# Performance work log

Hardware: AMD Instinct MI355X
Metric: run time of the kernel (lower is better)

## Reference

```python
import jax, jax.numpy as jnp
import numpy as np

EPS = 1e-8
NEG = -1e7  # min_val used by masked_max


def _div_safe(a, b):
    return a / jnp.maximum(b, EPS)


def _masked_max(v, m, axis):
    mb = jnp.broadcast_to(m, v.shape)
    val = jnp.where(mb > 0, v, NEG).max(axis=axis)
    return val * mb.max(axis=axis)


def _masked_mean(v, m, axis):
    mb = jnp.broadcast_to(m, v.shape)
    return _div_safe((v * mb).sum(axis=axis), mb.sum(axis=axis))


def _cos_pairwise(v1, v2):
    # v1: (b,p,h), v2: (b,q,h) -> (b,p,q)
    n1 = jnp.linalg.norm(v1, axis=2, keepdims=True)
    n2 = jnp.linalg.norm(v2, axis=2, keepdims=True)
    dot = jnp.einsum('bph,bqh->bpq', v1, v2)
    return _div_safe(dot, n1 * n2.transpose(0, 2, 1))


def _mpm(v1, v2, w):
    # v1,v2: (b,L,h); w: (np,h) -> ((b,L,1), (b,L,np))
    dot = (v1 * v2).sum(-1)
    n = jnp.linalg.norm(v1, axis=-1) * jnp.linalg.norm(v2, axis=-1)
    mv1 = _div_safe(dot, n)[..., None]
    wv1 = w[None, None] * v1[:, :, None, :]  # (b,L,np,h)
    wv2 = w[None, None] * v2[:, :, None, :]
    dotm = (wv1 * wv2).sum(-1)
    nm = jnp.linalg.norm(wv1, axis=-1) * jnp.linalg.norm(wv2, axis=-1)
    return mv1, _div_safe(dotm, nm)


def _mpm_pairwise(v1, v2, w):
    # v1: (b,L1,h), v2: (b,L2,h), w: (np,h) -> (b,L1,L2,np)
    wv1 = w[None, :, None, :] * v1[:, None, :, :]  # (b,np,L1,h)
    wv2 = w[None, :, None, :] * v2[:, None, :, :]  # (b,np,L2,h)
    n1 = jnp.linalg.norm(wv1, axis=3, keepdims=True)
    n2 = jnp.linalg.norm(wv2, axis=3, keepdims=True)
    dot = jnp.einsum('bnph,bnqh->bnpq', wv1, wv2)
    res = _div_safe(dot, n1 * n2.transpose(0, 1, 3, 2))
    return res.transpose(0, 2, 3, 1)


def _bimpm(context_p, mask_p, context_h, mask_h, w_full, w_maxpool, w_att, w_max_att):
    b = context_p.shape[0]
    mask_p_h = mask_p[:, :, None] * mask_h[:, None, :]  # (b,Lp,Lh)
    mask_h_p = mask_p_h.transpose(0, 2, 1)
    context_p = context_p * mask_p[:, :, None]
    context_h = context_h * mask_h[:, :, None]

    cos = _cos_pairwise(context_p, context_h)  # (b,Lp,Lh)
    mv_p = [_masked_max(cos, mask_p_h, 2)[:, :, None],
            _masked_mean(cos, mask_p_h, 2)[:, :, None]]
    cos_t = cos.transpose(0, 2, 1)
    mv_h = [_masked_max(cos_t, mask_h_p, 2)[:, :, None],
            _masked_mean(cos_t, mask_h_p, 2)[:, :, None]]

    # full match (is_forward=True): match against last non-pad token
    idx_p = jnp.clip(mask_p.sum(1).astype(jnp.int32) - 1, 0)
    idx_h = jnp.clip(mask_h.sum(1).astype(jnp.int32) - 1, 0)
    last_p = context_p[jnp.arange(b), idx_p][:, None, :]  # (b,1,h)
    last_h = context_h[jnp.arange(b), idx_h][:, None, :]
    m1, mm = _mpm(context_p, jnp.broadcast_to(last_h, context_p.shape), w_full)
    mv_p += [m1, mm]
    m1, mm = _mpm(context_h, jnp.broadcast_to(last_p, context_h.shape), w_full)
    mv_h += [m1, mm]

    # maxpool match
    mv_max = _mpm_pairwise(context_p, context_h, w_maxpool)  # (b,Lp,Lh,np)
    mv_p += [_masked_max(mv_max, mask_p_h[..., None], 2),
             _masked_mean(mv_max, mask_p_h[..., None], 2)]
    mv_max_t = mv_max.transpose(0, 2, 1, 3)
    mv_h += [_masked_max(mv_max_t, mask_h_p[..., None], 2),
             _masked_mean(mv_max_t, mask_h_p[..., None], 2)]

    # attentive match
    att_h = context_h[:, None, :, :] * cos[..., None]  # (b,Lp,Lh,h)
    att_p = context_p[:, :, None, :] * cos[..., None]  # (b,Lp,Lh,h)
    att_mean_h = _div_safe(jnp.einsum('bpq,bqh->bph', cos, context_h),
                           cos.sum(2, keepdims=True))
    att_mean_p = _div_safe(jnp.einsum('bpq,bph->bqh', cos, context_p),
                           cos.sum(1, keepdims=True).transpose(0, 2, 1))
    m1, mm = _mpm(context_p, att_mean_h, w_att)
    mv_p += [m1, mm]
    m1, mm = _mpm(context_h, att_mean_p, w_att)
    mv_h += [m1, mm]

    # max attentive match
    att_max_h = _masked_max(att_h, mask_p_h[..., None], 2)  # (b,Lp,h)
    att_max_p = _masked_max(att_p.transpose(0, 2, 1, 3), mask_h_p[..., None], 2)  # (b,Lh,h)
    m1, mm = _mpm(context_p, att_max_h, w_max_att)
    mv_p += [m1, mm]
    m1, mm = _mpm(context_h, att_max_p, w_max_att)
    mv_h += [m1, mm]

    return jnp.concatenate(mv_p, axis=2), jnp.concatenate(mv_h, axis=2)


def setup_inputs() -> dict:
    B, LP, LH, H, NP = 32, 128, 128, 200, 20
    key = jax.random.key(0)
    ks = jax.random.split(key, 8)
    len_p = jax.random.randint(ks[0], (B,), LP // 2, LP + 1)
    len_h = jax.random.randint(ks[1], (B,), LH // 2, LH + 1)
    return {
        'context_p': jax.random.normal(ks[2], (B, LP, H), dtype=jnp.float32),
        'mask_p': (jnp.arange(LP)[None, :] < len_p[:, None]).astype(jnp.float32),
        'context_h': jax.random.normal(ks[3], (B, LH, H), dtype=jnp.float32),
        'mask_h': (jnp.arange(LH)[None, :] < len_h[:, None]).astype(jnp.float32),
        'w_full': jax.random.uniform(ks[4], (NP, H), dtype=jnp.float32),
        'w_maxpool': jax.random.uniform(ks[5], (NP, H), dtype=jnp.float32),
        'w_att': jax.random.uniform(ks[6], (NP, H), dtype=jnp.float32),
        'w_max_att': jax.random.uniform(ks[7], (NP, H), dtype=jnp.float32),
    }


def reference(context_p, mask_p, context_h, mask_h, w_full, w_maxpool, w_att, w_max_att):
    return _bimpm(context_p, mask_p, context_h, mask_h, w_full, w_maxpool, w_att, w_max_att)
```

## Files before the change

### kernel.cpp

```cpp
#include <hip/hip_runtime.h>
#include <hip/hip_bf16.h>


#define EPSF 1e-8f
#define NEGF -1e7f

constexpr int Bc = 32, Lc = 128, Hc = 200, NPc = 20, NCHc = 105;
constexpr int KP = 224;
constexpr size_t SLH = (size_t)Bc * Lc * Hc;
constexpr size_t SLL = (size_t)Bc * Lc * Lc;

constexpr size_t OFF_CPM    = 0;
constexpr size_t OFF_CHM    = OFF_CPM + SLH;
constexpr size_t OFF_CHMT   = OFF_CHM + SLH;
constexpr size_t OFF_COS    = OFF_CHMT + SLH;
constexpr size_t OFF_COST   = OFF_COS + SLL;
constexpr size_t OFF_AMEANH = OFF_COST + SLL;
constexpr size_t OFF_AMAXH  = OFF_AMEANH + SLH;
constexpr size_t OFF_AMEANP = OFF_AMAXH + SLH;
constexpr size_t OFF_AMAXP  = OFF_AMEANP + SLH;
constexpr size_t OFF_NORMP  = OFF_AMAXP + SLH;
constexpr size_t OFF_NORMH  = OFF_NORMP + (size_t)Bc * Lc;
constexpr size_t OFF_LENP   = OFF_NORMH + (size_t)Bc * Lc;
constexpr size_t OFF_LENH   = OFF_LENP + Bc;
constexpr size_t OFF_LASTP  = OFF_LENH + Bc;
constexpr size_t OFF_LASTH  = OFF_LASTP + (size_t)Bc * Hc;
constexpr size_t OFF_NWP    = OFF_LASTH + (size_t)Bc * Hc;
constexpr size_t OFF_NWH    = OFF_NWP + (size_t)Bc * NPc * Lc;
constexpr size_t OFF_MASKPF = OFF_NWH + (size_t)Bc * NPc * Lc;
constexpr size_t OFF_MASKHF = OFF_MASKPF + (size_t)Bc * Lc;
constexpr size_t OFF_WFULL  = OFF_MASKHF + (size_t)Bc * Lc;
constexpr size_t OFF_WMP    = OFF_WFULL + (size_t)NPc * Hc;
constexpr size_t OFF_WATT   = OFF_WMP + (size_t)NPc * Hc;
constexpr size_t OFF_WMATT  = OFF_WATT + (size_t)NPc * Hc;
constexpr size_t OFF_FLAG   = OFF_WMATT + (size_t)NPc * Hc;
constexpr size_t OFF_WT     = OFF_FLAG + 64;
constexpr size_t OFF_RPMAX  = OFF_WT + (size_t)Hc * 64;
constexpr size_t OFF_RPSUM  = OFF_RPMAX + 2 * (size_t)Bc * NPc * Lc;
constexpr size_t OFF_CPMAX  = OFF_RPSUM + 2 * (size_t)Bc * NPc * Lc;
constexpr size_t OFF_CPSUM  = OFF_CPMAX + 2 * (size_t)Bc * NPc * Lc;
constexpr size_t OFF_CHB    = OFF_CPSUM + 2 * (size_t)Bc * NPc * Lc;
constexpr size_t OFF_CPB    = OFF_CHB + ((size_t)Bc * Lc * KP) / 2;
constexpr size_t OFF_W2K    = OFF_CPB + ((size_t)Bc * Lc * KP) / 2;
constexpr size_t WS_FLOATS  = OFF_W2K + (size_t)NPc * KP;

typedef __attribute__((ext_vector_type(8))) short short8v;
typedef __attribute__((ext_vector_type(4))) short short4v;
typedef __attribute__((ext_vector_type(4))) float float4v;

__device__ __forceinline__ float loadf(const void* p, size_t i, int isb) {
  if (isb) return __bfloat162float(((const __hip_bfloat16*)p)[i]);
  return ((const float*)p)[i];
}

__device__ __forceinline__ void storef(void* out, size_t i, float v, int isb) {
  if (isb) ((__hip_bfloat16*)out)[i] = __float2bfloat16(v);
  else ((float*)out)[i] = v;
}

__device__ __forceinline__ short b2s(float f) {
  __hip_bfloat16 h = __float2bfloat16(f);
  union { __hip_bfloat16 b; short s; } u;
  u.b = h;
  return u.s;
}

__device__ __forceinline__ short8v weight8(short8v a, float4v w0, float4v w1) {
  short8v r;
#pragma unroll
  for (int e = 0; e < 8; e++) {
    union { unsigned u; float f; } c;
    c.u = ((unsigned)(unsigned short)a[e]) << 16;
    float w = (e < 4) ? w0[e] : w1[e - 4];
    r[e] = b2s(c.f * w);
  }
  return r;
}

__global__ void convert_kernel(const void* cp_, const void* mp, const void* ch_,
                               const void* mh, const void* wf, const void* wmp,
                               const void* watt, const void* wma,
                               float* __restrict__ ws) {
  int isb = (((const unsigned short*)mp)[0] == 0x3F80u) ? 1 : 0;
  int bid = blockIdx.x;
  const int n0 = Bc * Lc;
  const int nw = NPc * Hc;
  if (bid >= 162) {
    int t = threadIdx.x;
    int idx = (bid - 162) * 4 + (t >> 6);
    int side = idx >> 5, b = idx & 31;
    int lane = t & 63;
    const void* mask = side ? mh : mp;
    const void* ctx = side ? ch_ : cp_;
    float s = 0.f;
    for (int l = lane; l < Lc; l += 64) s += loadf(mask, b * Lc + l, isb);
    for (int o = 32; o > 0; o >>= 1) s += __shfl_xor(s, o);
    if (lane == 0) ws[(side ? OFF_LENH : OFF_LENP) + b] = s;
    int lidx = (int)(s + 0.5f) - 1;
    if (lidx < 0) lidx = 0;
    float mk = loadf(mask, b * Lc + lidx, isb);
    float* lastv = ws + (side ? OFF_LASTH : OFF_LASTP) + (size_t)b * Hc;
    for (int h = lane; h < Hc; h += 64)
      lastv[h] = loadf(ctx, ((size_t)b * Lc + lidx) * Hc + h, isb) * mk;
    return;
  }
  int g = bid * 256 + threadIdx.x;
  if (g == 0) ws[OFF_FLAG] = (float)isb;
  if (g < n0) {
    ws[OFF_MASKPF + g] = loadf(mp, g, isb);
  } else if (g < 2 * n0) {
    ws[OFF_MASKHF + (g - n0)] = loadf(mh, g - n0, isb);
  } else if (g < 2 * n0 + 4 * nw) {
    int r = g - 2 * n0;
    int seg = r / nw, off = r % nw;
    if (seg == 0) ws[OFF_WFULL + off] = loadf(wf, off, isb);
    else if (seg == 1) ws[OFF_WMP + off] = loadf(wmp, off, isb);
    else if (seg == 2) ws[OFF_WATT + off] = loadf(watt, off, isb);
    else ws[OFF_WMATT + off] = loadf(wma, off, isb);
  } else if (g < 2 * n0 + 4 * nw + 64 * Hc) {
    int r = g - (2 * n0 + 4 * nw);
    int c = r / Hc, h = r % Hc;
    float w = 1.0f;
    if (c < 20) w = loadf(wf, (size_t)c * Hc + h, isb);
    else if (c < 40) w = loadf(watt, (size_t)(c - 20) * Hc + h, isb);
    else if (c < 60) w = loadf(wma, (size_t)(c - 40) * Hc + h, isb);
    ws[OFF_WT + r] = w * w;
  } else if (g < 2 * n0 + 4 * nw + 64 * Hc + NPc * KP) {
    int r = g - (2 * n0 + 4 * nw + 64 * Hc);
    int np_ = r / KP, k = r % KP;
    float w = (k < Hc) ? loadf(wmp, (size_t)np_ * Hc + k, isb) : 0.f;
    ws[OFF_W2K + r] = w * w;
  }
}

__global__ void prep_kernel(const void* __restrict__ ctx_p,
                            const void* __restrict__ ctx_h,
                            float* __restrict__ ws) {
  int bid = blockIdx.x;
  int side = bid >> 12;
  int bl = bid & 4095;
  int b = bl >> 7, l = bl & 127;
  int lane = threadIdx.x;
  int isb = ws[OFF_FLAG] > 0.5f;
  const void* ctx = side ? ctx_h : ctx_p;
  const float* mask = ws + (side ? OFF_MASKHF : OFF_MASKPF);
  float mk = mask[b * Lc + l];
  size_t rowbase = ((size_t)b * Lc + l) * Hc;
  float* cm = ws + (side ? OFF_CHM : OFF_CPM) + rowbase;
  __hip_bfloat16* cb16 = (__hip_bfloat16*)(ws + (side ? OFF_CHB : OFF_CPB));
  size_t cb = ((size_t)b * Lc + l) * KP;

  float v[4];
  float ss = 0.f;
  for (int i = 0; i < 4; i++) {
    int h = lane + 64 * i;
    float x = 0.f;
    if (h < Hc) {
      x = loadf(ctx, rowbase + h, isb) * mk;
      cm[h] = x;
      cb16[cb + h] = __float2bfloat16(x);
    } else if (h < KP) {
      cb16[cb + h] = __float2bfloat16(0.f);
    }
    v[i] = x;
    ss += x * x;
  }
  for (int o = 32; o > 0; o >>= 1) ss += __shfl_xor(ss, o);
  if (lane == 0) ws[(side ? OFF_NORMH : OFF_NORMP) + b * Lc + l] = sqrtf(ss);

  const float* wmpf = ws + OFF_WMP;
  float* nw = ws + (side ? OFF_NWH : OFF_NWP) + (size_t)b * NPc * Lc;
  for (int np_ = 0; np_ < NPc; np_++) {
    float s = 0.f;
    for (int i = 0; i < 4; i++) {
      int h = lane + 64 * i;
      if (h < Hc) {
        float w = wmpf[np_ * Hc + h];
        float wx = w * v[i];
        s += wx * wx;
      }
    }
    for (int o = 32; o > 0; o >>= 1) s += __shfl_xor(s, o);
    if (lane == 0) nw[np_ * Lc + l] = sqrtf(s);
  }
}

__global__ __launch_bounds__(64, 3) void maxpool_kernel(float* __restrict__ ws) {
  int s = blockIdx.x;
  int np_ = blockIdx.y, b = blockIdx.z;
  int pi = s >> 1, qi = s & 1;
  int cosmode = (np_ == NPc);
  int lane = threadIdx.x;
  int rsel = lane & 15, quad = lane >> 4;

  const short* Ab = (const short*)(ws + OFF_CPB)
                  + ((size_t)b * Lc + pi * 64 + rsel) * KP + quad * 8;
  const short* Bb = (const short*)(ws + OFF_CHB)
                  + ((size_t)b * Lc + qi * 64 + rsel) * KP + quad * 8;
  const float* w2k = ws + OFF_W2K + (size_t)(cosmode ? 0 : np_) * KP + quad * 8;

  float4v acc[4][4];
  float4v zf = {0.f, 0.f, 0.f, 0.f};
#pragma unroll
  for (int i = 0; i < 4; i++)
#pragma unroll
    for (int j = 0; j < 4; j++) acc[i][j] = zf;

#pragma unroll
  for (int st = 0; st < 7; st++) {
    int k0 = st * 32;
    short8v bf4[4], af[4];
#pragma unroll
    for (int t = 0; t < 4; t++)
      bf4[t] = *(const short8v*)(Bb + (size_t)t * 16 * KP + k0);
    if (cosmode) {
#pragma unroll
      for (int t = 0; t < 4; t++)
        af[t] = *(const short8v*)(Ab + (size_t)t * 16 * KP + k0);
    } else {
      float4v w0 = *(const float4v*)(w2k + k0);
      float4v w1 = *(const float4v*)(w2k + k0 + 4);
#pragma unroll
      for (int t = 0; t < 4; t++) {
        short8v ar = *(const short8v*)(Ab + (size_t)t * 16 * KP + k0);
        af[t] = weight8(ar, w0, w1);
      }
    }
#pragma unroll
    for (int i = 0; i < 4; i++)
#pragma unroll
      for (int j = 0; j < 4; j++)
        acc[i][j] = __builtin_amdgcn_mfma_f32_16x16x32_bf16(af[i], bf4[j], acc[i][j], 0, 0, 0);
  }

  if (cosmode) {
    const float* npn = ws + OFF_NORMP + b * Lc + pi * 64;
    const float* nhn = ws + OFF_NORMH + b * Lc + qi * 64;
    float nh4[4];
#pragma unroll
    for (int tj = 0; tj < 4; tj++) nh4[tj] = nhn[tj * 16 + rsel];
    float* cosp = ws + OFF_COS + (size_t)b * Lc * Lc;
    float* cost = ws + OFF_COST + (size_t)b * Lc * Lc;
#pragma unroll
    for (int ti = 0; ti < 4; ti++) {
#pragma unroll
      for (int r = 0; r < 4; r++) {
        int prow = pi * 64 + ti * 16 + quad * 4 + r;
        float npv = npn[ti * 16 + quad * 4 + r];
#pragma unroll
        for (int tj = 0; tj < 4; tj++) {
          int qcol = qi * 64 + tj * 16 + rsel;
          float v = acc[ti][tj][r] * __builtin_amdgcn_rcpf(fmaxf(npv * nh4[tj], EPSF));
          cosp[(size_t)prow * Lc + qcol] = v;
          cost[(size_t)qcol * Lc + prow] = v;
        }
      }
    }
    return;
  }

  const float* nwp = ws + OFF_NWP + ((size_t)b * NPc + np_) * Lc + pi * 64;
  const float* nwh = ws + OFF_NWH + ((size_t)b * NPc + np_) * Lc + qi * 64;
  const float* maskP = ws + OFF_MASKPF + b * Lc + pi * 64;
  const float* maskH = ws + OFF_MASKHF + b * Lc + qi * 64;
  float nhv[4], mhv[4], cmax[4], csum[4];
#pragma unroll
  for (int tj = 0; tj < 4; tj++) {
    int q = tj * 16 + rsel;
    nhv[tj] = nwh[q];
    mhv[tj] = maskH[q];
    cmax[tj] = NEGF;
    csum[tj] = 0.f;
  }
  size_t rbase = (((size_t)qi * Bc + b) * NPc + np_) * Lc + pi * 64;
  size_t cbase = (((size_t)pi * Bc + b) * NPc + np_) * Lc + qi * 64;
#pragma unroll
  for (int ti = 0; ti < 4; ti++) {
#pragma unroll
    for (int r = 0; r < 4; r++) {
      int p = ti * 16 + quad * 4 + r;
      float npv = nwp[p], mpv = maskP[p];
      float rm = NEGF, rs = 0.f;
#pragma unroll
      for (int tj = 0; tj < 4; tj++) {
        float v = acc[ti][tj][r] * __builtin_amdgcn_rcpf(fmaxf(npv * nhv[tj], EPSF));
        if (mhv[tj] > 0.f) rm = fmaxf(rm, v);
        rs += v * mhv[tj];
        if (mpv > 0.f) cmax[tj] = fmaxf(cmax[tj], v);
        csum[tj] += v * mpv;
      }
#pragma unroll
      for (int o = 1; o <= 8; o <<= 1) {
        rm = fmaxf(rm, __shfl_xor(rm, o));
        rs += __shfl_xor(rs, o);
      }
      if (rsel == 0) {
        ws[OFF_RPMAX + rbase + p] = rm;
        ws[OFF_RPSUM + rbase + p] = rs;
      }
    }
  }
#pragma unroll
  for (int tj = 0; tj < 4; tj++) {
#pragma unroll
    for (int o = 16; o <= 32; o <<= 1) {
      cmax[tj] = fmaxf(cmax[tj], __shfl_xor(cmax[tj], o));
      csum[tj] += __shfl_xor(csum[tj], o);
    }
  }
  if (quad == 0) {
#pragma unroll
    for (int tj = 0; tj < 4; tj++) {
      int q = tj * 16 + rsel;
      ws[OFF_CPMAX + cbase + q] = cmax[tj];
      ws[OFF_CPSUM + cbase + q] = csum[tj];
    }
  }
}

__global__ __launch_bounds__(256) void att_kernel(float* __restrict__ ws,
                                                  void* __restrict__ out) {
  int side = blockIdx.z;
  int b = blockIdx.y;
  int r0 = blockIdx.x * 4;
  int t = threadIdx.x;
  int isb = ws[OFF_FLAG] > 0.5f;
  const float* cosrows = ws + (side ? OFF_COST : OFF_COS) + ((size_t)b * Lc + r0) * Lc;
  const float* vsrc = ws + (side ? OFF_CPM : OFF_CHM) + (size_t)b * Lc * Hc;
  const float* maskLoop = ws + (side ? OFF_MASKPF : OFF_MASKHF) + b * Lc;
  const float* maskRow = ws + (side ? OFF_MASKHF : OFF_MASKPF) + b * Lc;
  float lenOther = ws[(side ? OFF_LENP : OFF_LENH) + b];
  float* amean = ws + (side ? OFF_AMEANP : OFF_AMEANH) + ((size_t)b * Lc + r0) * Hc;
  float* amax = ws + (side ? OFF_AMAXP : OFF_AMAXH) + ((size_t)b * Lc + r0) * Hc;

  __shared__ float crow[4][Lc];
  __shared__ float mneg[Lc];
  __shared__ float dens[4];
  for (int i = t; i < 4 * Lc; i += 256) crow[i >> 7][i & 127] = cosrows[i];
  if (t < Lc) mneg[t] = (maskLoop[t] > 0.f) ? 0.f : -1e30f;
  __syncthreads();

  int wv = t >> 6, lane = t & 63;
  {
    float x1 = crow[wv][lane], x2 = crow[wv][lane + 64];
    float sv = x1 + x2;
    float mv = fmaxf(x1 + mneg[lane], x2 + mneg[lane + 64]);
    for (int o = 32; o > 0; o >>= 1) {
      sv += __shfl_xor(sv, o);
      mv = fmaxf(mv, __shfl_xor(mv, o));
    }
    if (lane == 0) {
      dens[wv] = sv;
      float mr = maskRow[r0 + wv];
      size_t orow = (size_t)side * Bc * Lc * NCHc + ((size_t)b * Lc + r0 + wv) * NCHc;
      storef(out, orow + 0, mr * mv, isb);
      storef(out, orow + 1, mr * sv / fmaxf(mr * lenOther, EPSF), isb);
    }
  }
  __syncthreads();

  if (t < Hc) {
    float s0 = 0.f, s1 = 0.f, s2 = 0.f, s3 = 0.f;
    float m0 = NEGF, m1 = NEGF, m2 = NEGF, m3 = NEGF;
    const float* vb = vsrc + t;
#pragma unroll 4
    for (int q = 0; q < Lc; q++) {
      float pr = vb[(size_t)q * Hc];
      float mn = mneg[q];
      float v0 = crow[0][q] * pr; s0 += v0; m0 = fmaxf(m0, v0 + mn);
      float v1 = crow[1][q] * pr; s1 += v1; m1 = fmaxf(m1, v1 + mn);
      float v2 = crow[2][q] * pr; s2 += v2; m2 = fmaxf(m2, v2 + mn);
      float v3 = crow[3][q] * pr; s3 += v3; m3 = fmaxf(m3, v3 + mn);
    }
    amean[0 * Hc + t] = s0 / fmaxf(dens[0], EPSF);
    amean[1 * Hc + t] = s1 / fmaxf(dens[1], EPSF);
    amean[2 * Hc + t] = s2 / fmaxf(dens[2], EPSF);
    amean[3 * Hc + t] = s3 / fmaxf(dens[3], EPSF);
    amax[0 * Hc + t] = maskRow[r0 + 0] * m0;
    amax[1 * Hc + t] = maskRow[r0 + 1] * m1;
    amax[2 * Hc + t] = maskRow[r0 + 2] * m2;
    amax[3 * Hc + t] = maskRow[r0 + 3] * m3;
  }
}

__global__ __launch_bounds__(64) void mpm_kernel(float* __restrict__ ws,
                                                 void* __restrict__ out) {
  int bid = blockIdx.x;
  int side = bid >> 11;
  int b = (bid >> 6) & 31;
  int l0 = (bid & 63) * 2;
  int c = threadIdx.x;
  int isb = ws[OFF_FLAG] > 0.5f;
  __shared__ float v1s[2][Hc], v2l[Hc], v2a[2][Hc], v2m[2][Hc];
  const float* v1 = ws + (side ? OFF_CHM : OFF_CPM) + ((size_t)b * Lc + l0) * Hc;
  const float* vlast = ws + (side ? OFF_LASTP : OFF_LASTH) + (size_t)b * Hc;
  const float* va = ws + (side ? OFF_AMEANP : OFF_AMEANH) + ((size_t)b * Lc + l0) * Hc;
  const float* vm = ws + (side ? OFF_AMAXP : OFF_AMAXH) + ((size_t)b * Lc + l0) * Hc;
  for (int h = c; h < Hc; h += 64) {
    v1s[0][h] = v1[h];
    v1s[1][h] = v1[h + Hc];
    v2l[h] = vlast[h];
    v2a[0][h] = va[h];
    v2a[1][h] = va[h + Hc];
    v2m[0][h] = vm[h];
    v2m[1][h] = vm[h + Hc];
  }
  if (c < NPc) {
    size_t PMX = side ? OFF_CPMAX : OFF_RPMAX;
    size_t PSM = side ? OFF_CPSUM : OFF_RPSUM;
    float len = ws[(side ? OFF_LENP : OFF_LENH) + b];
#pragma unroll
    for (int l = 0; l < 2; l++) {
      size_t i0 = (((size_t)0 * Bc + b) * NPc + c) * Lc + l0 + l;
      size_t i1 = (((size_t)1 * Bc + b) * NPc + c) * Lc + l0 + l;
      float m = fmaxf(ws[PMX + i0], ws[PMX + i1]);
      float sum = ws[PSM + i0] + ws[PSM + i1];
      float mk = ws[(side ? OFF_MASKHF : OFF_MASKPF) + b * Lc + l0 + l];
      size_t orow = (size_t)side * Bc * Lc * NCHc + ((size_t)b * Lc + l0 + l) * NCHc;
      storef(out, orow + 23 + c, mk * m, isb);
      storef(out, orow + 43 + c, mk * sum / fmaxf(mk * len, EPSF), isb);
    }
  }
  __syncthreads();
  int v2i = (c < 20) ? 0 : (c < 40) ? 1 : (c < 60) ? 2 : (c - 60);
  if (v2i > 2) v2i = 2;
  const float* y0 = (v2i == 0) ? v2l : (v2i == 1) ? v2a[0] : v2m[0];
  const float* y1 = (v2i == 0) ? v2l : (v2i == 1) ? v2a[1] : v2m[1];
  const float* wt = ws + OFF_WT + (size_t)c * Hc;
  float sd0 = 0.f, sa0 = 0.f, sb0 = 0.f;
  float sd1 = 0.f, sa1 = 0.f, sb1 = 0.f;
#pragma unroll 2
  for (int h4 = 0; h4 < Hc / 4; h4++) {
    float4 wq = *(const float4*)(wt + h4 * 4);
    float4 x0 = *(const float4*)&v1s[0][h4 * 4];
    float4 x1 = *(const float4*)&v1s[1][h4 * 4];
    float4 ya = *(const float4*)&y0[h4 * 4];
    float4 yb = *(const float4*)&y1[h4 * 4];
    float t0;
    t0 = wq.x * x0.x; sd0 += t0 * ya.x; sa0 += t0 * x0.x; sb0 += wq.x * ya.x * ya.x;
    t0 = wq.y * x0.y; sd0 += t0 * ya.y; sa0 += t0 * x0.y; sb0 += wq.y * ya.y * ya.y;
    t0 = wq.z * x0.z; sd0 += t0 * ya.z; sa0 += t0 * x0.z; sb0 += wq.z * ya.z * ya.z;
    t0 = wq.w * x0.w; sd0 += t0 * ya.w; sa0 += t0 * x0.w; sb0 += wq.w * ya.w * ya.w;
    t0 = wq.x * x1.x; sd1 += t0 * yb.x; sa1 += t0 * x1.x; sb1 += wq.x * yb.x * yb.x;
    t0 = wq.y * x1.y; sd1 += t0 * yb.y; sa1 += t0 * x1.y; sb1 += wq.y * yb.y * yb.y;
    t0 = wq.z * x1.z; sd1 += t0 * yb.z; sa1 += t0 * x1.z; sb1 += wq.z * yb.z * yb.z;
    t0 = wq.w * x1.w; sd1 += t0 * yb.w; sa1 += t0 * x1.w; sb1 += wq.w * yb.w * yb.w;
  }
  float mm0 = sd0 / fmaxf(sqrtf(sa0) * sqrtf(sb0), EPSF);
  float mm1 = sd1 / fmaxf(sqrtf(sa1) * sqrtf(sb1), EPSF);
  int ch;
  if (c < 20) ch = 3 + c;
  else if (c < 40) ch = 64 + (c - 20);
  else if (c < 60) ch = 85 + (c - 40);
  else if (c == 60) ch = 2;
  else if (c == 61) ch = 63;
  else if (c == 62) ch = 84;
  else ch = -1;
  if (ch >= 0) {
    size_t orow = ((size_t)side * Bc * Lc + (size_t)b * Lc + l0) * NCHc;
    storef(out, orow + ch, mm0, isb);
    storef(out, orow + NCHc + ch, mm1, isb);
  }
}

extern "C" void kernel_launch(void* const* d_in, const int* in_sizes, int n_in,
                              void* d_out, int out_size, void* d_ws, size_t ws_size,
                              hipStream_t stream) {
  const void* ctx_p = d_in[0];
  const void* mask_p = d_in[1];
  const void* ctx_h = d_in[2];
  const void* mask_h = d_in[3];
  const void* w_full = d_in[4];
  const void* w_mp = d_in[5];
  const void* w_att = d_in[6];
  const void* w_maxatt = d_in[7];
  float* ws = (float*)d_ws;

  convert_kernel<<<178, 256, 0, stream>>>(ctx_p, mask_p, ctx_h, mask_h,
                                          w_full, w_mp, w_att, w_maxatt, ws);
  prep_kernel<<<2 * Bc * Lc, 64, 0, stream>>>(ctx_p, ctx_h, ws);
  maxpool_kernel<<<dim3(4, NPc + 1, Bc), 64, 0, stream>>>(ws);
  att_kernel<<<dim3(Lc / 4, Bc, 2), 256, 0, stream>>>(ws, d_out);
  mpm_kernel<<<2 * Bc * 64, 64, 0, stream>>>(ws, d_out);
}
```

Measured before the change: 188.7 us.

## Fuse convert with prep and attention with multi-perspective match kernels

After: 167.5 us. 11.2% less time.

```diff
diff --git a/kernel.cpp b/kernel.cpp
--- a/kernel.cpp
+++ b/kernel.cpp
@@ -12,14 +12,9 @@
 
 constexpr size_t OFF_CPM    = 0;
 constexpr size_t OFF_CHM    = OFF_CPM + SLH;
-constexpr size_t OFF_CHMT   = OFF_CHM + SLH;
-constexpr size_t OFF_COS    = OFF_CHMT + SLH;
+constexpr size_t OFF_COS    = OFF_CHM + SLH;
 constexpr size_t OFF_COST   = OFF_COS + SLL;
-constexpr size_t OFF_AMEANH = OFF_COST + SLL;
-constexpr size_t OFF_AMAXH  = OFF_AMEANH + SLH;
-constexpr size_t OFF_AMEANP = OFF_AMAXH + SLH;
-constexpr size_t OFF_AMAXP  = OFF_AMEANP + SLH;
-constexpr size_t OFF_NORMP  = OFF_AMAXP + SLH;
+constexpr size_t OFF_NORMP  = OFF_COST + SLL;
 constexpr size_t OFF_NORMH  = OFF_NORMP + (size_t)Bc * Lc;
 constexpr size_t OFF_LENP   = OFF_NORMH + (size_t)Bc * Lc;
 constexpr size_t OFF_LENH   = OFF_LENP + Bc;
@@ -29,11 +24,7 @@
 constexpr size_t OFF_NWH    = OFF_NWP + (size_t)Bc * NPc * Lc;
 constexpr size_t OFF_MASKPF = OFF_NWH + (size_t)Bc * NPc * Lc;
 constexpr size_t OFF_MASKHF = OFF_MASKPF + (size_t)Bc * Lc;
-constexpr size_t OFF_WFULL  = OFF_MASKHF + (size_t)Bc * Lc;
-constexpr size_t OFF_WMP    = OFF_WFULL + (size_t)NPc * Hc;
-constexpr size_t OFF_WATT   = OFF_WMP + (size_t)NPc * Hc;
-constexpr size_t OFF_WMATT  = OFF_WATT + (size_t)NPc * Hc;
-constexpr size_t OFF_FLAG   = OFF_WMATT + (size_t)NPc * Hc;
+constexpr size_t OFF_FLAG   = OFF_MASKHF + (size_t)Bc * Lc;
 constexpr size_t OFF_WT     = OFF_FLAG + 64;
 constexpr size_t OFF_RPMAX  = OFF_WT + (size_t)Hc * 64;
 constexpr size_t OFF_RPSUM  = OFF_RPMAX + 2 * (size_t)Bc * NPc * Lc;
@@ -45,7 +36,6 @@
 constexpr size_t WS_FLOATS  = OFF_W2K + (size_t)NPc * KP;
 
 typedef __attribute__((ext_vector_type(8))) short short8v;
-typedef __attribute__((ext_vector_type(4))) short short4v;
 typedef __attribute__((ext_vector_type(4))) float float4v;
 
 __device__ __forceinline__ float loadf(const void* p, size_t i, int isb) {
@@ -77,17 +67,67 @@
   return r;
 }
 
-__global__ void convert_kernel(const void* cp_, const void* mp, const void* ch_,
-                               const void* mh, const void* wf, const void* wmp,
-                               const void* watt, const void* wma,
-                               float* __restrict__ ws) {
+__global__ __launch_bounds__(256) void prep_kernel(
+    const void* __restrict__ cp_, const void* __restrict__ mp,
+    const void* __restrict__ ch_, const void* __restrict__ mh,
+    const void* __restrict__ wf, const void* __restrict__ wmp,
+    const void* __restrict__ watt, const void* __restrict__ wma,
+    float* __restrict__ ws) {
   int isb = (((const unsigned short*)mp)[0] == 0x3F80u) ? 1 : 0;
   int bid = blockIdx.x;
+  int t = threadIdx.x;
   const int n0 = Bc * Lc;
-  const int nw = NPc * Hc;
-  if (bid >= 162) {
-    int t = threadIdx.x;
-    int idx = (bid - 162) * 4 + (t >> 6);
+  if (bid < 2048) {
+    int g = bid * 4 + (t >> 6);
+    int side = g >> 12;
+    int bl = g & 4095;
+    int b = bl >> 7, l = bl & 127;
+    int lane = t & 63;
+    const void* ctx = side ? ch_ : cp_;
+    const void* maskin = side ? mh : mp;
+    float mk = loadf(maskin, b * Lc + l, isb);
+    size_t rowbase = ((size_t)b * Lc + l) * Hc;
+    float* cm = ws + (side ? OFF_CHM : OFF_CPM) + rowbase;
+    __hip_bfloat16* cb16 = (__hip_bfloat16*)(ws + (side ? OFF_CHB : OFF_CPB));
+    size_t cb = ((size_t)b * Lc + l) * KP;
+
+    float v[4];
+    float ss = 0.f;
+    for (int i = 0; i < 4; i++) {
+      int h = lane + 64 * i;
+      float x = 0.f;
+      if (h < Hc) {
+        x = loadf(ctx, rowbase + h, isb) * mk;
+        cm[h] = x;
+        cb16[cb + h] = __float2bfloat16(x);
+      } else if (h < KP) {
+        cb16[cb + h] = __float2bfloat16(0.f);
+      }
+      v[i] = x;
+      ss += x * x;
+    }
+    for (int o = 32; o > 0; o >>= 1) ss += __shfl_xor(ss, o);
+    if (lane == 0) ws[(side ? OFF_NORMH : OFF_NORMP) + b * Lc + l] = sqrtf(ss);
+
+    float* nw = ws + (side ? OFF_NWH : OFF_NWP) + (size_t)b * NPc * Lc;
+    for (int np_ = 0; np_ < NPc; np_++) {
+      float s = 0.f;
+      for (int i = 0; i < 4; i++) {
+        int h = lane + 64 * i;
+        if (h < Hc) {
+          float w = loadf(wmp, (size_t)np_ * Hc + h, isb);
+          float wx = w * v[i];
+          s += wx * wx;
+        }
+      }
+      for (int o = 32; o > 0; o >>= 1) s += __shfl_xor(s, o);
+      if (lane == 0) nw[np_ * Lc + l] = sqrtf(s);
+    }
+    return;
+  }
+  int cb = bid - 2048;
+  if (cb >= 100) {
+    int idx = (cb - 100) * 4 + (t >> 6);
     int side = idx >> 5, b = idx & 31;
     int lane = t & 63;
     const void* mask = side ? mh : mp;
@@ -104,84 +144,25 @@
       lastv[h] = loadf(ctx, ((size_t)b * Lc + lidx) * Hc + h, isb) * mk;
     return;
   }
-  int g = bid * 256 + threadIdx.x;
+  int g = cb * 256 + t;
   if (g == 0) ws[OFF_FLAG] = (float)isb;
   if (g < n0) {
     ws[OFF_MASKPF + g] = loadf(mp, g, isb);
   } else if (g < 2 * n0) {
     ws[OFF_MASKHF + (g - n0)] = loadf(mh, g - n0, isb);
-  } else if (g < 2 * n0 + 4 * nw) {
+  } else if (g < 2 * n0 + 64 * Hc) {
     int r = g - 2 * n0;
-    int seg = r / nw, off = r % nw;
-    if (seg == 0) ws[OFF_WFULL + off] = loadf(wf, off, isb);
-    else if (seg == 1) ws[OFF_WMP + off] = loadf(wmp, off, isb);
-    else if (seg == 2) ws[OFF_WATT + off] = loadf(watt, off, isb);
-    else ws[OFF_WMATT + off] = loadf(wma, off, isb);
-  } else if (g < 2 * n0 + 4 * nw + 64 * Hc) {
-    int r = g - (2 * n0 + 4 * nw);
     int c = r / Hc, h = r % Hc;
     float w = 1.0f;
     if (c < 20) w = loadf(wf, (size_t)c * Hc + h, isb);
     else if (c < 40) w = loadf(watt, (size_t)(c - 20) * Hc + h, isb);
     else if (c < 60) w = loadf(wma, (size_t)(c - 40) * Hc + h, isb);
     ws[OFF_WT + r] = w * w;
-  } else if (g < 2 * n0 + 4 * nw + 64 * Hc + NPc * KP) {
-    int r = g - (2 * n0 + 4 * nw + 64 * Hc);
+  } else if (g < 2 * n0 + 64 * Hc + NPc * KP) {
+    int r = g - (2 * n0 + 64 * Hc);
     int np_ = r / KP, k = r % KP;
     float w = (k < Hc) ? loadf(wmp, (size_t)np_ * Hc + k, isb) : 0.f;
     ws[OFF_W2K + r] = w * w;
-  }
-}
-
-__global__ void prep_kernel(const void* __restrict__ ctx_p,
-                            const void* __restrict__ ctx_h,
-                            float* __restrict__ ws) {
-  int bid = blockIdx.x;
-  int side = bid >> 12;
-  int bl = bid & 4095;
-  int b = bl >> 7, l = bl & 127;
-  int lane = threadIdx.x;
-  int isb = ws[OFF_FLAG] > 0.5f;
-  const void* ctx = side ? ctx_h : ctx_p;
-  const float* mask = ws + (side ? OFF_MASKHF : OFF_MASKPF);
-  float mk = mask[b * Lc + l];
-  size_t rowbase = ((size_t)b * Lc + l) * Hc;
-  float* cm = ws + (side ? OFF_CHM : OFF_CPM) + rowbase;
-  __hip_bfloat16* cb16 = (__hip_bfloat16*)(ws + (side ? OFF_CHB : OFF_CPB));
-  size_t cb = ((size_t)b * Lc + l) * KP;
-
-  float v[4];
-  float ss = 0.f;
-  for (int i = 0; i < 4; i++) {
-    int h = lane + 64 * i;
-    float x = 0.f;
-    if (h < Hc) {
-      x = loadf(ctx, rowbase + h, isb) * mk;
-      cm[h] = x;
-      cb16[cb + h] = __float2bfloat16(x);
-    } else if (h < KP) {
-      cb16[cb + h] = __float2bfloat16(0.f);
-    }
-    v[i] = x;
-    ss += x * x;
-  }
-  for (int o = 32; o > 0; o >>= 1) ss += __shfl_xor(ss, o);
-  if (lane == 0) ws[(side ? OFF_NORMH : OFF_NORMP) + b * Lc + l] = sqrtf(ss);
-
-  const float* wmpf = ws + OFF_WMP;
-  float* nw = ws + (side ? OFF_NWH : OFF_NWP) + (size_t)b * NPc * Lc;
-  for (int np_ = 0; np_ < NPc; np_++) {
-    float s = 0.f;
-    for (int i = 0; i < 4; i++) {
-      int h = lane + 64 * i;
-      if (h < Hc) {
-        float w = wmpf[np_ * Hc + h];
-        float wx = w * v[i];
-        s += wx * wx;
-      }
-    }
-    for (int o = 32; o > 0; o >>= 1) s += __shfl_xor(s, o);
-    if (lane == 0) nw[np_ * Lc + l] = sqrtf(s);
   }
 }
 
@@ -318,8 +299,8 @@
   }
 }
 
-__global__ __launch_bounds__(256) void att_kernel(float* __restrict__ ws,
-                                                  void* __restrict__ out) {
+__global__ __launch_bounds__(256) void attmpm_kernel(float* __restrict__ ws,
+                                                     void* __restrict__ out) {
   int side = blockIdx.z;
   int b = blockIdx.y;
   int r0 = blockIdx.x * 4;
@@ -327,17 +308,24 @@
   int isb = ws[OFF_FLAG] > 0.5f;
   const float* cosrows = ws + (side ? OFF_COST : OFF_COS) + ((size_t)b * Lc + r0) * Lc;
   const float* vsrc = ws + (side ? OFF_CPM : OFF_CHM) + (size_t)b * Lc * Hc;
+  const float* v1g = ws + (side ? OFF_CHM : OFF_CPM) + ((size_t)b * Lc + r0) * Hc;
+  const float* vlast = ws + (side ? OFF_LASTP : OFF_LASTH) + (size_t)b * Hc;
   const float* maskLoop = ws + (side ? OFF_MASKPF : OFF_MASKHF) + b * Lc;
   const float* maskRow = ws + (side ? OFF_MASKHF : OFF_MASKPF) + b * Lc;
   float lenOther = ws[(side ? OFF_LENP : OFF_LENH) + b];
-  float* amean = ws + (side ? OFF_AMEANP : OFF_AMEANH) + ((size_t)b * Lc + r0) * Hc;
-  float* amax = ws + (side ? OFF_AMAXP : OFF_AMAXH) + ((size_t)b * Lc + r0) * Hc;
+  size_t obase = (size_t)side * Bc * Lc * NCHc + ((size_t)b * Lc + r0) * NCHc;
 
   __shared__ float crow[4][Lc];
   __shared__ float mneg[Lc];
   __shared__ float dens[4];
+  __shared__ float v1s[4][Hc];
+  __shared__ float v2l[Hc];
+  __shared__ float am[4][Hc];
+  __shared__ float ax[4][Hc];
   for (int i = t; i < 4 * Lc; i += 256) crow[i >> 7][i & 127] = cosrows[i];
   if (t < Lc) mneg[t] = (maskLoop[t] > 0.f) ? 0.f : -1e30f;
+  for (int i = t; i < 4 * Hc; i += 256) v1s[i / Hc][i % Hc] = v1g[i];
+  for (int h = t; h < Hc; h += 256) v2l[h] = vlast[h];
   __syncthreads();
 
   int wv = t >> 6, lane = t & 63;
@@ -352,9 +340,8 @@
     if (lane == 0) {
       dens[wv] = sv;
       float mr = maskRow[r0 + wv];
-      size_t orow = (size_t)side * Bc * Lc * NCHc + ((size_t)b * Lc + r0 + wv) * NCHc;
-      storef(out, orow + 0, mr * mv, isb);
-      storef(out, orow + 1, mr * sv / fmaxf(mr * lenOther, EPSF), isb);
+      storef(out, obase + (size_t)wv * NCHc + 0, mr * mv, isb);
+      storef(out, obase + (size_t)wv * NCHc + 1, mr * sv / fmaxf(mr * lenOther, EPSF), isb);
     }
   }
   __syncthreads();
@@ -372,82 +359,51 @@
       float v2 = crow[2][q] * pr; s2 += v2; m2 = fmaxf(m2, v2 + mn);
       float v3 = crow[3][q] * pr; s3 += v3; m3 = fmaxf(m3, v3 + mn);
     }
-    amean[0 * Hc + t] = s0 / fmaxf(dens[0], EPSF);
-    amean[1 * Hc + t] = s1 / fmaxf(dens[1], EPSF);
-    amean[2 * Hc + t] = s2 / fmaxf(dens[2], EPSF);
-    amean[3 * Hc + t] = s3 / fmaxf(dens[3], EPSF);
-    amax[0 * Hc + t] = maskRow[r0 + 0] * m0;
-    amax[1 * Hc + t] = maskRow[r0 + 1] * m1;
-    amax[2 * Hc + t] = maskRow[r0 + 2] * m2;
-    amax[3 * Hc + t] = maskRow[r0 + 3] * m3;
-  }
-}
-
-__global__ __launch_bounds__(64) void mpm_kernel(float* __restrict__ ws,
-                                                 void* __restrict__ out) {
-  int bid = blockIdx.x;
-  int side = bid >> 11;
-  int b = (bid >> 6) & 31;
-  int l0 = (bid & 63) * 2;
-  int c = threadIdx.x;
-  int isb = ws[OFF_FLAG] > 0.5f;
-  __shared__ float v1s[2][Hc], v2l[Hc], v2a[2][Hc], v2m[2][Hc];
-  const float* v1 = ws + (side ? OFF_CHM : OFF_CPM) + ((size_t)b * Lc + l0) * Hc;
-  const float* vlast = ws + (side ? OFF_LASTP : OFF_LASTH) + (size_t)b * Hc;
-  const float* va = ws + (side ? OFF_AMEANP : OFF_AMEANH) + ((size_t)b * Lc + l0) * Hc;
-  const float* vm = ws + (side ? OFF_AMAXP : OFF_AMAXH) + ((size_t)b * Lc + l0) * Hc;
-  for (int h = c; h < Hc; h += 64) {
-    v1s[0][h] = v1[h];
-    v1s[1][h] = v1[h + Hc];
-    v2l[h] = vlast[h];
-    v2a[0][h] = va[h];
-    v2a[1][h] = va[h + Hc];
-    v2m[0][h] = vm[h];
-    v2m[1][h] = vm[h + Hc];
-  }
+    am[0][t] = s0 / fmaxf(dens[0], EPSF);
+    am[1][t] = s1 / fmaxf(dens[1], EPSF);
+    am[2][t] = s2 / fmaxf(dens[2], EPSF);
+    am[3][t] = s3 / fmaxf(dens[3], EPSF);
+    ax[0][t] = maskRow[r0 + 0] * m0;
+    ax[1][t] = maskRow[r0 + 1] * m1;
+    ax[2][t] = maskRow[r0 + 2] * m2;
+    ax[3][t] = maskRow[r0 + 3] * m3;
+  }
+  __syncthreads();
+
+  int c = lane;
+  int row = r0 + wv;
+  size_t orow = obase + (size_t)wv * NCHc;
+
   if (c < NPc) {
     size_t PMX = side ? OFF_CPMAX : OFF_RPMAX;
     size_t PSM = side ? OFF_CPSUM : OFF_RPSUM;
-    float len = ws[(side ? OFF_LENP : OFF_LENH) + b];
-#pragma unroll
-    for (int l = 0; l < 2; l++) {
-      size_t i0 = (((size_t)0 * Bc + b) * NPc + c) * Lc + l0 + l;
-      size_t i1 = (((size_t)1 * Bc + b) * NPc + c) * Lc + l0 + l;
-      float m = fmaxf(ws[PMX + i0], ws[PMX + i1]);
-      float sum = ws[PSM + i0] + ws[PSM + i1];
-      float mk = ws[(side ? OFF_MASKHF : OFF_MASKPF) + b * Lc + l0 + l];
-      size_t orow = (size_t)side * Bc * Lc * NCHc + ((size_t)b * Lc + l0 + l) * NCHc;
-      storef(out, orow + 23 + c, mk * m, isb);
-      storef(out, orow + 43 + c, mk * sum / fmaxf(mk * len, EPSF), isb);
-    }
-  }
-  __syncthreads();
+    size_t i0 = (((size_t)0 * Bc + b) * NPc + c) * Lc + row;
+    size_t i1 = (((size_t)1 * Bc + b) * NPc + c) * Lc + row;
+    float m = fmaxf(ws[PMX + i0], ws[PMX + i1]);
+    float sum = ws[PSM + i0] + ws[PSM + i1];
+    float mk = maskRow[row];
+    storef(out, orow + 23 + c, mk * m, isb);
+    storef(out, orow + 43 + c, mk * sum / fmaxf(mk * lenOther, EPSF), isb);
+  }
+
   int v2i = (c < 20) ? 0 : (c < 40) ? 1 : (c < 60) ? 2 : (c - 60);
   if (v2i > 2) v2i = 2;
-  const float* y0 = (v2i == 0) ? v2l : (v2i == 1) ? v2a[0] : v2m[0];
-  const float* y1 = (v2i == 0) ? v2l : (v2i == 1) ? v2a[1] : v2m[1];
+  const float* y = (v2i == 0) ? v2l : (v2i == 1) ? am[wv] : ax[wv];
+  const float* x = v1s[wv];
   const float* wt = ws + OFF_WT + (size_t)c * Hc;
-  float sd0 = 0.f, sa0 = 0.f, sb0 = 0.f;
-  float sd1 = 0.f, sa1 = 0.f, sb1 = 0.f;
+  float sd = 0.f, sa = 0.f, sb = 0.f;
 #pragma unroll 2
   for (int h4 = 0; h4 < Hc / 4; h4++) {
     float4 wq = *(const float4*)(wt + h4 * 4);
-    float4 x0 = *(const float4*)&v1s[0][h4 * 4];
-    float4 x1 = *(const float4*)&v1s[1][h4 * 4];
-    float4 ya = *(const float4*)&y0[h4 * 4];
-    float4 yb = *(const float4*)&y1[h4 * 4];
+    float4 xv = *(const float4*)&x[h4 * 4];
+    float4 yv = *(const float4*)&y[h4 * 4];
     float t0;
-    t0 = wq.x * x0.x; sd0 += t0 * ya.x; sa0 += t0 * x0.x; sb0 += wq.x * ya.x * ya.x;
-    t0 = wq.y * x0.y; sd0 += t0 * ya.y; sa0 += t0 * x0.y; sb0 += wq.y * ya.y * ya.y;
-    t0 = wq.z * x0.z; sd0 += t0 * ya.z; sa0 += t0 * x0.z; sb0 += wq.z * ya.z * ya.z;
-    t0 = wq.w * x0.w; sd0 += t0 * ya.w; sa0 += t0 * x0.w; sb0 += wq.w * ya.w * ya.w;
-    t0 = wq.x * x1.x; sd1 += t0 * yb.x; sa1 += t0 * x1.x; sb1 += wq.x * yb.x * yb.x;
-    t0 = wq.y * x1.y; sd1 += t0 * yb.y; sa1 += t0 * x1.y; sb1 += wq.y * yb.y * yb.y;
-    t0 = wq.z * x1.z; sd1 += t0 * yb.z; sa1 += t0 * x1.z; sb1 += wq.z * yb.z * yb.z;
-    t0 = wq.w * x1.w; sd1 += t0 * yb.w; sa1 += t0 * x1.w; sb1 += wq.w * yb.w * yb.w;
-  }
-  float mm0 = sd0 / fmaxf(sqrtf(sa0) * sqrtf(sb0), EPSF);
-  float mm1 = sd1 / fmaxf(sqrtf(sa1) * sqrtf(sb1), EPSF);
+    t0 = wq.x * xv.x; sd += t0 * yv.x; sa += t0 * xv.x; sb += wq.x * yv.x * yv.x;
+    t0 = wq.y * xv.y; sd += t0 * yv.y; sa += t0 * xv.y; sb += wq.y * yv.y * yv.y;
+    t0 = wq.z * xv.z; sd += t0 * yv.z; sa += t0 * xv.z; sb += wq.z * yv.z * yv.z;
+    t0 = wq.w * xv.w; sd += t0 * yv.w; sa += t0 * xv.w; sb += wq.w * yv.w * yv.w;
+  }
+  float mm = sd / fmaxf(sqrtf(sa) * sqrtf(sb), EPSF);
   int ch;
   if (c < 20) ch = 3 + c;
   else if (c < 40) ch = 64 + (c - 20);
@@ -456,11 +412,7 @@
   else if (c == 61) ch = 63;
   else if (c == 62) ch = 84;
   else ch = -1;
-  if (ch >= 0) {
-    size_t orow = ((size_t)side * Bc * Lc + (size_t)b * Lc + l0) * NCHc;
-    storef(out, orow + ch, mm0, isb);
-    storef(out, orow + NCHc + ch, mm1, isb);
-  }
+  if (ch >= 0) storef(out, orow + ch, mm, isb);
 }
 
 extern "C" void kernel_launch(void* const* d_in, const int* in_sizes, int n_in,
@@ -476,10 +428,8 @@
   const void* w_maxatt = d_in[7];
   float* ws = (float*)d_ws;
 
-  convert_kernel<<<178, 256, 0, stream>>>(ctx_p, mask_p, ctx_h, mask_h,
-                                          w_full, w_mp, w_att, w_maxatt, ws);
-  prep_kernel<<<2 * Bc * Lc, 64, 0, stream>>>(ctx_p, ctx_h, ws);
+  prep_kernel<<<2164, 256, 0, stream>>>(ctx_p, mask_p, ctx_h, mask_h,
+                                        w_full, w_mp, w_att, w_maxatt, ws);
   maxpool_kernel<<<dim3(4, NPc + 1, Bc), 64, 0, stream>>>(ws);
-  att_kernel<<<dim3(Lc / 4, Bc, 2), 256, 0, stream>>>(ws, d_out);
-  mpm_kernel<<<2 * Bc * 64, 64, 0, stream>>>(ws, d_out);
-}
+  attmpm_kernel<<<dim3(Lc / 4, Bc, 2), 256, 0, stream>>>(ws, d_out);
+}
```
